# Kernel tuning notes

Hardware: AMD Instinct MI355X
Metric: run time of the kernel (lower is better)

## Reference

```python
import jax, jax.numpy as jnp
import numpy as np

D_MODEL = 1024
EXPAND = 2
D_INNER = D_MODEL * EXPAND  # 2048 independent SSM channels
D_STATE = 16
BATCH = 4
SEQ = 4096


def setup_inputs() -> dict:
    key = jax.random.key(0)
    ks = jax.random.split(key, 10)
    w = lambda k, shape, scale=0.02: jax.random.normal(k, shape, jnp.float32) * scale
    return {
        "x": jax.random.normal(ks[0], (BATCH, SEQ, D_MODEL), jnp.float32),
        "w_in": w(ks[1], (D_MODEL, D_INNER)),
        "b_in": jnp.zeros((D_INNER,), jnp.float32),
        "w_gate": w(ks[2], (D_MODEL, D_INNER)),
        "b_gate": jnp.zeros((D_INNER,), jnp.float32),
        # per-channel linear SSM params: h_t = A h_{t-1} + B x_t ; y_t = C . h_t
        "A": w(ks[3], (D_INNER, D_STATE, D_STATE), 0.05),  # small spectral radius -> stable recurrence
        "B_ssm": w(ks[4], (D_INNER, D_STATE), 0.1),
        "C_ssm": w(ks[5], (D_INNER, D_STATE), 0.1),
        "w_out": w(ks[6], (D_INNER, D_MODEL)),
        "b_out": jnp.zeros((D_MODEL,), jnp.float32),
    }


def reference(x, w_in, b_in, w_gate, b_gate, A, B_ssm, C_ssm, w_out, b_out):
    # x: [B, S, D]
    x_proj = x @ w_in + b_in                     # [B, S, C]
    gate = jax.nn.sigmoid(x @ w_gate + b_gate)   # [B, S, C]

    def step(h, xt):
        # h: [B, C, N] state for all channels; xt: [B, C] scalar input per channel
        h = jnp.einsum("cnm,bcm->bcn", A, h) + B_ssm[None] * xt[:, :, None]
        y = jnp.einsum("bcn,cn->bc", h, C_ssm)
        return h, y

    h0 = jnp.zeros((x.shape[0], D_INNER, D_STATE), x.dtype)
    xs = jnp.swapaxes(x_proj, 0, 1)              # [S, B, C]
    _, ys = jax.lax.scan(step, h0, xs)           # ys: [S, B, C]
    ssm_out = jnp.swapaxes(ys, 0, 1)             # [B, S, C]

    y = ssm_out * gate
    return y @ w_out + b_out                     # [B, S, D]
```

## Files before the change

### kernel.cpp

```cpp
#include <hip/hip_runtime.h>
#include <hip/hip_bf16.h>

#define D_MODEL 1024
#define D_INNER 2048
#define D_STATE 16
#define BATCH   4
#define SEQ     4096
#define MROWS   (BATCH * SEQ)

#define LTAPS 16
#define TSPAN 64

using bf16 = __hip_bfloat16;

typedef __attribute__((ext_vector_type(8))) short bf16x8;
typedef __attribute__((ext_vector_type(4))) float f32x4;

__device__ __forceinline__ float bf2f(bf16 v) { return __bfloat162float(v); }
__device__ __forceinline__ unsigned short f2bfbits(float f) {
  bf16 h = __float2bfloat16(f);
  return *(unsigned short*)&h;
}
__device__ __forceinline__ float bfbits2f(unsigned short u) {
  union { float f; unsigned int i; } x; x.i = (unsigned int)u << 16; return x.f;
}

#define AS1CAST(p) ((const __attribute__((address_space(1))) unsigned int*)(unsigned long long)(p))
#define AS3CAST(p) ((__attribute__((address_space(3))) unsigned int*)(unsigned long long)(p))

#define TILE_E 16384

struct G4 {
  const bf16 *gA, *gB;
  int sW;
  int baseA0, baseA1;
  int baseB0, baseB1;
  int wr, wc, lane;
};

template<int KK>
__device__ __forceinline__ void g4_setup(G4& g, const bf16* A, const bf16* BT,
                                         int m0, int n0)
{
  const int tid = threadIdx.x;
  g.lane = tid & 63;
  const int wv = tid >> 6;
  g.wr = wv >> 1;
  g.wc = wv & 1;
  const int lr = g.lane >> 3, sl = g.lane & 7;
  g.gA = A  + (size_t)(m0 + wv * 64 + lr) * KK + (sl ^ lr) * 8;
  g.gB = BT + (size_t)(n0 + wv * 64 + lr) * KK + (sl ^ lr) * 8;
  g.sW = wv * 4096;
  const int fla = g.lane & 15, cb = g.lane >> 4;
  const int s0 = cb ^ (fla & 7);
  g.baseA0 = (g.wr * 128 + fla) * 64 + s0 * 8;
  g.baseA1 = (g.wr * 128 + fla) * 64 + (s0 ^ 4) * 8;
  g.baseB0 = (g.wc * 128 + fla) * 64 + s0 * 8;
  g.baseB1 = (g.wc * 128 + fla) * 64 + (s0 ^ 4) * 8;
}

template<int KK>
__device__ __forceinline__ void g4_stage(const bf16* s, bf16* d)
{
#pragma unroll
  for (int i = 0; i < 8; ++i)
    __builtin_amdgcn_global_load_lds(AS1CAST(s + (size_t)i * 8 * KK),
                                     AS3CAST(d + i * 512), 16, 0, 0);
}

__device__ __forceinline__ void rd8(bf16x8 (&d)[8], const bf16* T, int base)
{
#pragma unroll
  for (int i = 0; i < 8; ++i)
    d[i] = *(const bf16x8*)&T[base + i * 1024];
}

#define CL64(AF, BF) do { _Pragma("unroll") \
  for (int mi = 0; mi < 8; ++mi) { _Pragma("unroll") \
    for (int ni = 0; ni < 8; ++ni) \
      acc[mi][ni] = __builtin_amdgcn_mfma_f32_16x16x32_bf16( \
          (AF)[mi], (BF)[ni], acc[mi][ni], 0, 0, 0); \
  } } while (0)

template<int KK, int CUR, bool MORE>
__device__ __forceinline__ void g4_tile(const G4& g, bf16* As, bf16* Bs, int t,
    f32x4 (&acc)[8][8],
    bf16x8 (&a0)[8], bf16x8 (&b0)[8], bf16x8 (&a1)[8], bf16x8 (&b1)[8])
{
  const bf16* Ac = As + CUR * TILE_E;
  const bf16* Bc = Bs + CUR * TILE_E;
  rd8(a1, Ac, g.baseA1);
  rd8(b1, Bc, g.baseB1);
  if constexpr (MORE) {
    g4_stage<KK>(g.gA + (size_t)(t + 1) * 64, As + (CUR ^ 1) * TILE_E + g.sW);
    g4_stage<KK>(g.gB + (size_t)(t + 1) * 64, Bs + (CUR ^ 1) * TILE_E + g.sW);
  }
  __builtin_amdgcn_sched_barrier(0);
  CL64(a0, b0);
  __builtin_amdgcn_sched_barrier(0);
  asm volatile("s_waitcnt lgkmcnt(0)" ::: "memory");
  if constexpr (MORE) {
    asm volatile("s_waitcnt vmcnt(0)" ::: "memory");
    __builtin_amdgcn_s_barrier();
    rd8(a0, As + (CUR ^ 1) * TILE_E, g.baseA0);
    rd8(b0, Bs + (CUR ^ 1) * TILE_E, g.baseB0);
  }
  __builtin_amdgcn_sched_barrier(0);
  CL64(a1, b1);
}

template<int KK>
__device__ __forceinline__ void g4_main(const G4& g, bf16* As, bf16* Bs,
                                        f32x4 (&acc)[8][8])
{
  const int nt = KK >> 6;
  g4_stage<KK>(g.gA, As + g.sW);
  g4_stage<KK>(g.gB, Bs + g.sW);
  asm volatile("s_waitcnt vmcnt(0)" ::: "memory");
  __builtin_amdgcn_s_barrier();

  bf16x8 a0[8], b0[8], a1[8], b1[8];
  rd8(a0, As, g.baseA0);
  rd8(b0, Bs, g.baseB0);

  for (int t = 0; t < nt - 2; t += 2) {
    g4_tile<KK, 0, true>(g, As, Bs, t,     acc, a0, b0, a1, b1);
    g4_tile<KK, 1, true>(g, As, Bs, t + 1, acc, a0, b0, a1, b1);
  }
  g4_tile<KK, 0, true >(g, As, Bs, nt - 2, acc, a0, b0, a1, b1);
  g4_tile<KK, 1, false>(g, As, Bs, nt - 1, acc, a0, b0, a1, b1);
}

__global__ __launch_bounds__(256, 1) void gemm_proj_dual(
    const bf16* __restrict__ A,
    const bf16* __restrict__ BT,
    const float* __restrict__ bias_in, const float* __restrict__ bias_gate,
    bf16* __restrict__ xp, bf16* __restrict__ gate)
{
  __shared__ alignas(16) bf16 As[2 * TILE_E];
  __shared__ alignas(16) bf16 Bs[2 * TILE_E];

  const int b = blockIdx.x;
  const int swz = (b & 7) * 128 + (b >> 3);
  const int bm = swz >> 4, bn = swz & 15;
  const int m0 = bm * 256, n0 = bn * 256;

  G4 g;
  g4_setup<D_MODEL>(g, A, BT, m0, n0);

  f32x4 acc[8][8];
#pragma unroll
  for (int i = 0; i < 8; ++i)
#pragma unroll
    for (int j = 0; j < 8; ++j) acc[i][j] = (f32x4){0.f, 0.f, 0.f, 0.f};

  g4_main<D_MODEL>(g, As, Bs, acc);

  const bool isGate = (n0 >= D_INNER);
  const int  nloc0  = n0 - (isGate ? D_INNER : 0);
  const float* bias = isGate ? bias_gate : bias_in;
  bf16* dst         = isGate ? gate : xp;

  const int crow = (g.lane >> 4) * 4;
  const int ccol = g.lane & 15;
#pragma unroll
  for (int mi = 0; mi < 8; ++mi)
#pragma unroll
    for (int ni = 0; ni < 8; ++ni) {
      const int col = nloc0 + g.wc * 128 + ni * 16 + ccol;
      const float bcol = bias[col];
#pragma unroll
      for (int r = 0; r < 4; ++r) {
        const size_t row = (size_t)(m0 + g.wr * 128 + mi * 16 + crow + r);
        float v = acc[mi][ni][r] + bcol;
        if (isGate) v = 1.0f / (1.0f + __expf(-v));
        dst[row * D_INNER + col] = __float2bfloat16(v);
      }
    }
}

__global__ __launch_bounds__(256, 1) void gemm_out(
    const bf16* __restrict__ A,
    const bf16* __restrict__ BT,
    const float* __restrict__ bias,
    float* __restrict__ C)
{
  __shared__ alignas(16) bf16 As[2 * TILE_E];
  __shared__ alignas(16) bf16 Bs[2 * TILE_E];

  const int b = blockIdx.x;
  const int swz = (b & 7) * 32 + (b >> 3);
  const int bm = swz >> 2, bn = swz & 3;
  const int m0 = bm * 256, n0 = bn * 256;

  G4 g;
  g4_setup<D_INNER>(g, A, BT, m0, n0);

  f32x4 acc[8][8];
#pragma unroll
  for (int i = 0; i < 8; ++i)
#pragma unroll
    for (int j = 0; j < 8; ++j) acc[i][j] = (f32x4){0.f, 0.f, 0.f, 0.f};

  g4_main<D_INNER>(g, As, Bs, acc);

  const int crow = (g.lane >> 4) * 4;
  const int ccol = g.lane & 15;
#pragma unroll
  for (int mi = 0; mi < 8; ++mi)
#pragma unroll
    for (int ni = 0; ni < 8; ++ni) {
      const int col = n0 + g.wc * 128 + ni * 16 + ccol;
      const float bcol = bias[col];
#pragma unroll
      for (int r = 0; r < 4; ++r) {
        const size_t row = (size_t)(m0 + g.wr * 128 + mi * 16 + crow + r);
        C[row * D_MODEL + col] = acc[mi][ni][r] + bcol;
      }
    }
}

__global__ __launch_bounds__(256) void f32_to_bf16(
    const float* __restrict__ in, bf16* __restrict__ out, int n4)
{
  const int i = (blockIdx.x * 256 + threadIdx.x);
  if (i >= n4) return;
  const float4 v = *(const float4*)(in + (size_t)i * 4);
  ushort4 r;
  r.x = f2bfbits(v.x); r.y = f2bfbits(v.y); r.z = f2bfbits(v.z); r.w = f2bfbits(v.w);
  *(ushort4*)(out + (size_t)i * 4) = r;
}

__global__ __launch_bounds__(256) void transpose_to_bf16(
    const float* __restrict__ in, bf16* __restrict__ out, int R, int C)
{
  __shared__ float tile[32][33];
  const int c0 = blockIdx.x * 32, r0 = blockIdx.y * 32;
  const int tx = threadIdx.x & 31, ty = threadIdx.x >> 5;
#pragma unroll
  for (int i = ty; i < 32; i += 8)
    tile[i][tx] = in[(size_t)(r0 + i) * C + c0 + tx];
  __syncthreads();
#pragma unroll
  for (int i = ty; i < 32; i += 8)
    out[(size_t)(c0 + i) * R + r0 + tx] = __float2bfloat16(tile[tx][i]);
}

__device__ __forceinline__ float4 load4f(const float* p) { return *(const float4*)p; }

__global__ __launch_bounds__(256) void ssm_taps(
    const float* __restrict__ A, const float* __restrict__ Bv,
    const float* __restrict__ Cv, float* __restrict__ g)
{
  const int c = blockIdx.x * blockDim.x + threadIdx.x;
  if (c >= D_INNER) return;
  const float* Ac = A + (size_t)c * D_STATE * D_STATE;
  float v[D_STATE], cr[D_STATE];
#pragma unroll
  for (int i = 0; i < D_STATE; ++i) {
    v[i]  = Bv[(size_t)c * D_STATE + i];
    cr[i] = Cv[(size_t)c * D_STATE + i];
  }
  for (int m = 0; m < LTAPS; ++m) {
    float y = 0.f;
#pragma unroll
    for (int i = 0; i < D_STATE; ++i) y += cr[i] * v[i];
    g[(size_t)m * D_INNER + c] = y;
    float nv[D_STATE];
#pragma unroll
    for (int n = 0; n < D_STATE; ++n) {
      const float4 a0 = load4f(Ac + n * D_STATE + 0);
      const float4 a1 = load4f(Ac + n * D_STATE + 4);
      const float4 a2 = load4f(Ac + n * D_STATE + 8);
      const float4 a3 = load4f(Ac + n * D_STATE + 12);
      float s = a0.x * v[0] + a0.y * v[1] + a0.z * v[2] + a0.w * v[3];
      s += a1.x * v[4] + a1.y * v[5] + a1.z * v[6] + a1.w * v[7];
      s += a2.x * v[8] + a2.y * v[9] + a2.z * v[10] + a2.w * v[11];
      s += a3.x * v[12] + a3.y * v[13] + a3.z * v[14] + a3.w * v[15];
      nv[n] = s;
    }
#pragma unroll
    for (int i = 0; i < D_STATE; ++i) v[i] = nv[i];
  }
}

__global__ __launch_bounds__(256) void conv_gate(
    const bf16* __restrict__ xp, bf16* __restrict__ gate_io,
    const float* __restrict__ g)
{
  const int cp = blockIdx.x * blockDim.x + threadIdx.x;
  const int c  = cp * 2;
  const int b  = blockIdx.z;
  const int t0 = blockIdx.y * TSPAN;

  float gg0[LTAPS], gg1[LTAPS];
#pragma unroll
  for (int m = 0; m < LTAPS; ++m) {
    gg0[m] = g[(size_t)m * D_INNER + c];
    gg1[m] = g[(size_t)m * D_INNER + c + 1];
  }

  const size_t baseBC = ((size_t)b * SEQ) * D_INNER + c;

  float w0[2 * LTAPS], w1[2 * LTAPS];
#pragma unroll
  for (int j = 0; j < LTAPS; ++j) {
    const int t = t0 - LTAPS + j;
    if (t >= 0) {
      const ushort2 v = *(const ushort2*)&xp[baseBC + (size_t)t * D_INNER];
      w0[j] = bfbits2f(v.x); w1[j] = bfbits2f(v.y);
    } else { w0[j] = 0.f; w1[j] = 0.f; }
  }

  for (int blk = 0; blk < TSPAN; blk += LTAPS) {
#pragma unroll
    for (int j = 0; j < LTAPS; ++j) {
      const ushort2 v = *(const ushort2*)&xp[baseBC + (size_t)(t0 + blk + j) * D_INNER];
      w0[LTAPS + j] = bfbits2f(v.x); w1[LTAPS + j] = bfbits2f(v.y);
    }
#pragma unroll
    for (int j = 0; j < LTAPS; ++j) {
      float y0 = 0.f, y1 = 0.f;
#pragma unroll
      for (int m = 0; m < LTAPS; ++m) {
        y0 += gg0[m] * w0[LTAPS + j - m];
        y1 += gg1[m] * w1[LTAPS + j - m];
      }
      const size_t idx = baseBC + (size_t)(t0 + blk + j) * D_INNER;
      const unsigned int gv = *(const unsigned int*)&gate_io[idx];
      const float g0 = bfbits2f((unsigned short)(gv & 0xffffu));
      const float g1 = bfbits2f((unsigned short)(gv >> 16));
      const unsigned int ov =
          (unsigned int)f2bfbits(y0 * g0) | ((unsigned int)f2bfbits(y1 * g1) << 16);
      *(unsigned int*)&gate_io[idx] = ov;
    }
#pragma unroll
    for (int j = 0; j < LTAPS; ++j) { w0[j] = w0[j + LTAPS]; w1[j] = w1[j + LTAPS]; }
  }
}

extern "C" void kernel_launch(void* const* d_in, const int* in_sizes, int n_in,
                              void* d_out, int out_size, void* d_ws, size_t ws_size,
                              hipStream_t stream)
{
  const float* x      = (const float*)d_in[0];
  const float* w_in   = (const float*)d_in[1];
  const float* b_in   = (const float*)d_in[2];
  const float* w_gate = (const float*)d_in[3];
  const float* b_gate = (const float*)d_in[4];
  const float* A      = (const float*)d_in[5];
  const float* B_ssm  = (const float*)d_in[6];
  const float* C_ssm  = (const float*)d_in[7];
  const float* w_out  = (const float*)d_in[8];
  const float* b_out  = (const float*)d_in[9];
  float* out = (float*)d_out;

  char* ws = (char*)d_ws;
  bf16*  gate  = (bf16*)(ws);
  bf16*  xbf   = (bf16*)(ws + 67108864);
  bf16*  wcatT = (bf16*)(ws + 100663296);
  bf16*  w_otT = (bf16*)(ws + 109051904);
  float* taps  = (float*)(ws + 113246208);
  bf16*  xp    = (bf16*)d_out;

  dim3 blk(256);

  hipLaunchKernelGGL(ssm_taps, dim3(D_INNER / 256), blk, 0, stream, A, B_ssm, C_ssm, taps);
  hipLaunchKernelGGL(f32_to_bf16, dim3((MROWS * D_MODEL / 4) / 256), blk, 0, stream,
                     x, xbf, MROWS * D_MODEL / 4);
  hipLaunchKernelGGL(transpose_to_bf16, dim3(D_INNER / 32, D_MODEL / 32), blk, 0, stream,
                     w_in, wcatT, D_MODEL, D_INNER);
  hipLaunchKernelGGL(transpose_to_bf16, dim3(D_INNER / 32, D_MODEL / 32), blk, 0, stream,
                     w_gate, wcatT + (size_t)D_INNER * D_MODEL, D_MODEL, D_INNER);
  hipLaunchKernelGGL(transpose_to_bf16, dim3(D_MODEL / 32, D_INNER / 32), blk, 0, stream,
                     w_out, w_otT, D_INNER, D_MODEL);

  dim3 gblk(256);
  hipLaunchKernelGGL(gemm_proj_dual, dim3((2 * D_INNER / 256) * (MROWS / 256)), gblk, 0, stream,
                     xbf, wcatT, b_in, b_gate, xp, gate);

  dim3 gc(D_INNER / 2 / 256, SEQ / TSPAN, BATCH);
  hipLaunchKernelGGL(conv_gate, gc, blk, 0, stream, xp, gate, taps);

  hipLaunchKernelGGL(gemm_out, dim3((D_MODEL / 256) * (MROWS / 256)), gblk, 0, stream,
                     gate, w_otT, b_out, out);
}
```

Baseline: 471.5 us.

## Switch GEMMs to 32x32x16 MFMA with 8 waves and fuse prep kernels

Both GEMMs are rewritten to use 512-thread blocks (8 waves, 2x4 layout), each wave computing a 128x64 sub-tile with 32x32x16 bf16 MFMA instead of 16x16x32. The K-tile is split into four 16-wide sub-steps with register double-buffering, and s_setprio is raised around MFMA clusters. The five prep kernels (x cast, three weight transposes, SSM taps) are merged into one launch. The aim is fewer LDS reads per FLOP, more waves to hide latency, and less launch overhead, at the cost of new register and occupancy tradeoffs (launch bounds 512,2) and a new fragment layout in the epilogue.

```diff
diff --git a/kernel.cpp b/kernel.cpp
--- a/kernel.cpp
+++ b/kernel.cpp
@@ -13,8 +13,8 @@
 
 using bf16 = __hip_bfloat16;
 
-typedef __attribute__((ext_vector_type(8))) short bf16x8;
-typedef __attribute__((ext_vector_type(4))) float f32x4;
+typedef __attribute__((ext_vector_type(8)))  short bf16x8;
+typedef __attribute__((ext_vector_type(16))) float f32x16;
 
 __device__ __forceinline__ float bf2f(bf16 v) { return __bfloat162float(v); }
 __device__ __forceinline__ unsigned short f2bfbits(float f) {
@@ -28,110 +28,133 @@
 #define AS1CAST(p) ((const __attribute__((address_space(1))) unsigned int*)(unsigned long long)(p))
 #define AS3CAST(p) ((__attribute__((address_space(3))) unsigned int*)(unsigned long long)(p))
 
+#define PRIO1 __builtin_amdgcn_s_setprio(1)
+#define PRIO0 __builtin_amdgcn_s_setprio(0)
+#define SBAR0 __builtin_amdgcn_sched_barrier(0)
+
 #define TILE_E 16384
 
-struct G4 {
+struct G32 {
   const bf16 *gA, *gB;
+  size_t K64, K128;
   int sW;
-  int baseA0, baseA1;
-  int baseB0, baseB1;
-  int wr, wc, lane;
+  int offA[4], offB[4];
+  int wm, wn, lane;
 };
 
 template<int KK>
-__device__ __forceinline__ void g4_setup(G4& g, const bf16* A, const bf16* BT,
-                                         int m0, int n0)
+__device__ __forceinline__ void g32_setup(G32& g, const bf16* A, const bf16* BT,
+                                          int m0, int n0)
 {
   const int tid = threadIdx.x;
   g.lane = tid & 63;
   const int wv = tid >> 6;
-  g.wr = wv >> 1;
-  g.wc = wv & 1;
+  g.wm = wv >> 2;
+  g.wn = wv & 3;
   const int lr = g.lane >> 3, sl = g.lane & 7;
-  g.gA = A  + (size_t)(m0 + wv * 64 + lr) * KK + (sl ^ lr) * 8;
-  g.gB = BT + (size_t)(n0 + wv * 64 + lr) * KK + (sl ^ lr) * 8;
-  g.sW = wv * 4096;
-  const int fla = g.lane & 15, cb = g.lane >> 4;
-  const int s0 = cb ^ (fla & 7);
-  g.baseA0 = (g.wr * 128 + fla) * 64 + s0 * 8;
-  g.baseA1 = (g.wr * 128 + fla) * 64 + (s0 ^ 4) * 8;
-  g.baseB0 = (g.wc * 128 + fla) * 64 + s0 * 8;
-  g.baseB1 = (g.wc * 128 + fla) * 64 + (s0 ^ 4) * 8;
-}
-
-template<int KK>
-__device__ __forceinline__ void g4_stage(const bf16* s, bf16* d)
-{
-#pragma unroll
-  for (int i = 0; i < 8; ++i)
-    __builtin_amdgcn_global_load_lds(AS1CAST(s + (size_t)i * 8 * KK),
-                                     AS3CAST(d + i * 512), 16, 0, 0);
-}
-
-__device__ __forceinline__ void rd8(bf16x8 (&d)[8], const bf16* T, int base)
-{
-#pragma unroll
-  for (int i = 0; i < 8; ++i)
-    d[i] = *(const bf16x8*)&T[base + i * 1024];
-}
-
-#define CL64(AF, BF) do { _Pragma("unroll") \
-  for (int mi = 0; mi < 8; ++mi) { _Pragma("unroll") \
-    for (int ni = 0; ni < 8; ++ni) \
-      acc[mi][ni] = __builtin_amdgcn_mfma_f32_16x16x32_bf16( \
-          (AF)[mi], (BF)[ni], acc[mi][ni], 0, 0, 0); \
+  g.gA = A  + (size_t)(m0 + wv * 8 + lr) * KK + (sl ^ lr) * 8;
+  g.gB = BT + (size_t)(n0 + wv * 8 + lr) * KK + (sl ^ lr) * 8;
+  g.K64  = (size_t)64 * KK;
+  g.K128 = (size_t)128 * KK;
+  g.sW = wv * 8 * 64;
+  const int l31 = g.lane & 31, hi = g.lane >> 5;
+#pragma unroll
+  for (int ks = 0; ks < 4; ++ks) {
+    const int slot = ((ks * 2 + hi) ^ (l31 & 7)) * 8;
+    g.offA[ks] = (g.wm * 128 + l31) * 64 + slot;
+    g.offB[ks] = (g.wn * 64  + l31) * 64 + slot;
+  }
+}
+
+__device__ __forceinline__ void g32_stage2(const bf16* s, bf16* d, size_t K64)
+{
+  __builtin_amdgcn_global_load_lds(AS1CAST(s),       AS3CAST(d),        16, 0, 0);
+  __builtin_amdgcn_global_load_lds(AS1CAST(s + K64), AS3CAST(d + 4096), 16, 0, 0);
+}
+
+__device__ __forceinline__ void rdA32(bf16x8 (&d)[4], const bf16* T, int off)
+{
+#pragma unroll
+  for (int am = 0; am < 4; ++am) d[am] = *(const bf16x8*)&T[off + am * 2048];
+}
+__device__ __forceinline__ void rdB32(bf16x8 (&d)[2], const bf16* T, int off)
+{
+#pragma unroll
+  for (int bn = 0; bn < 2; ++bn) d[bn] = *(const bf16x8*)&T[off + bn * 2048];
+}
+
+#define CL8(AF, BF) do { _Pragma("unroll") \
+  for (int am = 0; am < 4; ++am) { _Pragma("unroll") \
+    for (int bn = 0; bn < 2; ++bn) \
+      acc[am][bn] = __builtin_amdgcn_mfma_f32_32x32x16_bf16( \
+          (AF)[am], (BF)[bn], acc[am][bn], 0, 0, 0); \
   } } while (0)
 
-template<int KK, int CUR, bool MORE>
-__device__ __forceinline__ void g4_tile(const G4& g, bf16* As, bf16* Bs, int t,
-    f32x4 (&acc)[8][8],
-    bf16x8 (&a0)[8], bf16x8 (&b0)[8], bf16x8 (&a1)[8], bf16x8 (&b1)[8])
-{
-  const bf16* Ac = As + CUR * TILE_E;
-  const bf16* Bc = Bs + CUR * TILE_E;
-  rd8(a1, Ac, g.baseA1);
-  rd8(b1, Bc, g.baseB1);
+template<bool MORE>
+__device__ __forceinline__ void g32_tile(const G32& g, bf16* As, bf16* Bs, int t,
+    f32x16 (&acc)[4][2], bf16x8 (&aC)[4], bf16x8 (&bC)[2],
+    bf16x8 (&aN)[4], bf16x8 (&bN)[2])
+{
+  const int cur = t & 1;
+  const bf16* Ac = As + cur * TILE_E;
+  const bf16* Bc = Bs + cur * TILE_E;
+  bf16* Anx = As + (cur ^ 1) * TILE_E;
+  bf16* Bnx = Bs + (cur ^ 1) * TILE_E;
+
+  rdA32(aN, Ac, g.offA[1]);
+  rdB32(bN, Bc, g.offB[1]);
   if constexpr (MORE) {
-    g4_stage<KK>(g.gA + (size_t)(t + 1) * 64, As + (CUR ^ 1) * TILE_E + g.sW);
-    g4_stage<KK>(g.gB + (size_t)(t + 1) * 64, Bs + (CUR ^ 1) * TILE_E + g.sW);
-  }
-  __builtin_amdgcn_sched_barrier(0);
-  CL64(a0, b0);
-  __builtin_amdgcn_sched_barrier(0);
-  asm volatile("s_waitcnt lgkmcnt(0)" ::: "memory");
+    const size_t tau = (size_t)(t + 1) * 64;
+    g32_stage2(g.gA + tau,           Anx + g.sW,        g.K64);
+    g32_stage2(g.gA + g.K128 + tau,  Anx + 8192 + g.sW, g.K64);
+    g32_stage2(g.gB + tau,           Bnx + g.sW,        g.K64);
+    g32_stage2(g.gB + g.K128 + tau,  Bnx + 8192 + g.sW, g.K64);
+  }
+  SBAR0;
+  PRIO1; CL8(aC, bC); PRIO0;
+  rdA32(aC, Ac, g.offA[2]);
+  rdB32(bC, Bc, g.offB[2]);
+  SBAR0;
+  PRIO1; CL8(aN, bN); PRIO0;
+  rdA32(aN, Ac, g.offA[3]);
+  rdB32(bN, Bc, g.offB[3]);
+  SBAR0;
+  PRIO1; CL8(aC, bC); PRIO0;
   if constexpr (MORE) {
+    asm volatile("s_waitcnt lgkmcnt(0)" ::: "memory");
     asm volatile("s_waitcnt vmcnt(0)" ::: "memory");
     __builtin_amdgcn_s_barrier();
-    rd8(a0, As + (CUR ^ 1) * TILE_E, g.baseA0);
-    rd8(b0, Bs + (CUR ^ 1) * TILE_E, g.baseB0);
-  }
-  __builtin_amdgcn_sched_barrier(0);
-  CL64(a1, b1);
+  }
+  SBAR0;
+  PRIO1; CL8(aN, bN); PRIO0;
+  if constexpr (MORE) {
+    rdA32(aC, Anx, g.offA[0]);
+    rdB32(bC, Bnx, g.offB[0]);
+  }
 }
 
 template<int KK>
-__device__ __forceinline__ void g4_main(const G4& g, bf16* As, bf16* Bs,
-                                        f32x4 (&acc)[8][8])
+__device__ __forceinline__ void g32_main(const G32& g, bf16* As, bf16* Bs,
+                                         f32x16 (&acc)[4][2])
 {
   const int nt = KK >> 6;
-  g4_stage<KK>(g.gA, As + g.sW);
-  g4_stage<KK>(g.gB, Bs + g.sW);
+  g32_stage2(g.gA,           As + g.sW,        g.K64);
+  g32_stage2(g.gA + g.K128,  As + 8192 + g.sW, g.K64);
+  g32_stage2(g.gB,           Bs + g.sW,        g.K64);
+  g32_stage2(g.gB + g.K128,  Bs + 8192 + g.sW, g.K64);
   asm volatile("s_waitcnt vmcnt(0)" ::: "memory");
   __builtin_amdgcn_s_barrier();
 
-  bf16x8 a0[8], b0[8], a1[8], b1[8];
-  rd8(a0, As, g.baseA0);
-  rd8(b0, Bs, g.baseB0);
-
-  for (int t = 0; t < nt - 2; t += 2) {
-    g4_tile<KK, 0, true>(g, As, Bs, t,     acc, a0, b0, a1, b1);
-    g4_tile<KK, 1, true>(g, As, Bs, t + 1, acc, a0, b0, a1, b1);
-  }
-  g4_tile<KK, 0, true >(g, As, Bs, nt - 2, acc, a0, b0, a1, b1);
-  g4_tile<KK, 1, false>(g, As, Bs, nt - 1, acc, a0, b0, a1, b1);
-}
-
-__global__ __launch_bounds__(256, 1) void gemm_proj_dual(
+  bf16x8 aC[4], bC[2], aN[4], bN[2];
+  rdA32(aC, As, g.offA[0]);
+  rdB32(bC, Bs, g.offB[0]);
+
+  for (int t = 0; t < nt - 1; ++t)
+    g32_tile<true>(g, As, Bs, t, acc, aC, bC, aN, bN);
+  g32_tile<false>(g, As, Bs, nt - 1, acc, aC, bC, aN, bN);
+}
+
+__global__ __launch_bounds__(512, 2) void gemm_proj_dual(
     const bf16* __restrict__ A,
     const bf16* __restrict__ BT,
     const float* __restrict__ bias_in, const float* __restrict__ bias_gate,
@@ -145,41 +168,43 @@
   const int bm = swz >> 4, bn = swz & 15;
   const int m0 = bm * 256, n0 = bn * 256;
 
-  G4 g;
-  g4_setup<D_MODEL>(g, A, BT, m0, n0);
-
-  f32x4 acc[8][8];
-#pragma unroll
-  for (int i = 0; i < 8; ++i)
-#pragma unroll
-    for (int j = 0; j < 8; ++j) acc[i][j] = (f32x4){0.f, 0.f, 0.f, 0.f};
-
-  g4_main<D_MODEL>(g, As, Bs, acc);
+  G32 g;
+  g32_setup<D_MODEL>(g, A, BT, m0, n0);
+
+  f32x16 acc[4][2];
+#pragma unroll
+  for (int i = 0; i < 4; ++i)
+#pragma unroll
+    for (int j = 0; j < 2; ++j)
+#pragma unroll
+      for (int r = 0; r < 16; ++r) acc[i][j][r] = 0.f;
+
+  g32_main<D_MODEL>(g, As, Bs, acc);
 
   const bool isGate = (n0 >= D_INNER);
   const int  nloc0  = n0 - (isGate ? D_INNER : 0);
   const float* bias = isGate ? bias_gate : bias_in;
   bf16* dst         = isGate ? gate : xp;
 
-  const int crow = (g.lane >> 4) * 4;
-  const int ccol = g.lane & 15;
-#pragma unroll
-  for (int mi = 0; mi < 8; ++mi)
-#pragma unroll
-    for (int ni = 0; ni < 8; ++ni) {
-      const int col = nloc0 + g.wc * 128 + ni * 16 + ccol;
+  const int l31 = g.lane & 31, hi = g.lane >> 5;
+#pragma unroll
+  for (int am = 0; am < 4; ++am)
+#pragma unroll
+    for (int bn2 = 0; bn2 < 2; ++bn2) {
+      const int col = nloc0 + g.wn * 64 + bn2 * 32 + l31;
       const float bcol = bias[col];
 #pragma unroll
-      for (int r = 0; r < 4; ++r) {
-        const size_t row = (size_t)(m0 + g.wr * 128 + mi * 16 + crow + r);
-        float v = acc[mi][ni][r] + bcol;
+      for (int reg = 0; reg < 16; ++reg) {
+        const int rowl = (reg & 3) + 8 * (reg >> 2) + 4 * hi;
+        const size_t row = (size_t)(m0 + g.wm * 128 + am * 32 + rowl);
+        float v = acc[am][bn2][reg] + bcol;
         if (isGate) v = 1.0f / (1.0f + __expf(-v));
         dst[row * D_INNER + col] = __float2bfloat16(v);
       }
     }
 }
 
-__global__ __launch_bounds__(256, 1) void gemm_out(
+__global__ __launch_bounds__(512, 2) void gemm_out(
     const bf16* __restrict__ A,
     const bf16* __restrict__ BT,
     const float* __restrict__ bias,
@@ -193,49 +218,43 @@
   const int bm = swz >> 2, bn = swz & 3;
   const int m0 = bm * 256, n0 = bn * 256;
 
-  G4 g;
-  g4_setup<D_INNER>(g, A, BT, m0, n0);
-
-  f32x4 acc[8][8];
-#pragma unroll
-  for (int i = 0; i < 8; ++i)
-#pragma unroll
-    for (int j = 0; j < 8; ++j) acc[i][j] = (f32x4){0.f, 0.f, 0.f, 0.f};
-
-  g4_main<D_INNER>(g, As, Bs, acc);
-
-  const int crow = (g.lane >> 4) * 4;
-  const int ccol = g.lane & 15;
-#pragma unroll
-  for (int mi = 0; mi < 8; ++mi)
-#pragma unroll
-    for (int ni = 0; ni < 8; ++ni) {
-      const int col = n0 + g.wc * 128 + ni * 16 + ccol;
+  G32 g;
+  g32_setup<D_INNER>(g, A, BT, m0, n0);
+
+  f32x16 acc[4][2];
+#pragma unroll
+  for (int i = 0; i < 4; ++i)
+#pragma unroll
+    for (int j = 0; j < 2; ++j)
+#pragma unroll
+      for (int r = 0; r < 16; ++r) acc[i][j][r] = 0.f;
+
+  g32_main<D_INNER>(g, As, Bs, acc);
+
+  const int l31 = g.lane & 31, hi = g.lane >> 5;
+#pragma unroll
+  for (int am = 0; am < 4; ++am)
+#pragma unroll
+    for (int bn2 = 0; bn2 < 2; ++bn2) {
+      const int col = n0 + g.wn * 64 + bn2 * 32 + l31;
       const float bcol = bias[col];
 #pragma unroll
-      for (int r = 0; r < 4; ++r) {
-        const size_t row = (size_t)(m0 + g.wr * 128 + mi * 16 + crow + r);
-        C[row * D_MODEL + col] = acc[mi][ni][r] + bcol;
+      for (int reg = 0; reg < 16; ++reg) {
+        const int rowl = (reg & 3) + 8 * (reg >> 2) + 4 * hi;
+        const size_t row = (size_t)(m0 + g.wm * 128 + am * 32 + rowl);
+        C[row * D_MODEL + col] = acc[am][bn2][reg] + bcol;
       }
     }
 }
 
-__global__ __launch_bounds__(256) void f32_to_bf16(
-    const float* __restrict__ in, bf16* __restrict__ out, int n4)
-{
-  const int i = (blockIdx.x * 256 + threadIdx.x);
-  if (i >= n4) return;
-  const float4 v = *(const float4*)(in + (size_t)i * 4);
-  ushort4 r;
-  r.x = f2bfbits(v.x); r.y = f2bfbits(v.y); r.z = f2bfbits(v.z); r.w = f2bfbits(v.w);
-  *(ushort4*)(out + (size_t)i * 4) = r;
-}
-
-__global__ __launch_bounds__(256) void transpose_to_bf16(
-    const float* __restrict__ in, bf16* __restrict__ out, int R, int C)
-{
-  __shared__ float tile[32][33];
-  const int c0 = blockIdx.x * 32, r0 = blockIdx.y * 32;
+__device__ __forceinline__ float4 load4f(const float* p) { return *(const float4*)p; }
+
+__device__ __forceinline__ void transpose_body(
+    const float* __restrict__ in, bf16* __restrict__ out, int R, int C,
+    int idx, float (*tile)[33])
+{
+  const int nbx = C / 32;
+  const int c0 = (idx % nbx) * 32, r0 = (idx / nbx) * 32;
   const int tx = threadIdx.x & 31, ty = threadIdx.x >> 5;
 #pragma unroll
   for (int i = ty; i < 32; i += 8)
@@ -246,41 +265,61 @@
     out[(size_t)(c0 + i) * R + r0 + tx] = __float2bfloat16(tile[tx][i]);
 }
 
-__device__ __forceinline__ float4 load4f(const float* p) { return *(const float4*)p; }
-
-__global__ __launch_bounds__(256) void ssm_taps(
+__global__ __launch_bounds__(256) void prep_all(
+    const float* __restrict__ x,
+    const float* __restrict__ w_in, const float* __restrict__ w_gate,
+    const float* __restrict__ w_out,
     const float* __restrict__ A, const float* __restrict__ Bv,
-    const float* __restrict__ Cv, float* __restrict__ g)
-{
-  const int c = blockIdx.x * blockDim.x + threadIdx.x;
-  if (c >= D_INNER) return;
-  const float* Ac = A + (size_t)c * D_STATE * D_STATE;
-  float v[D_STATE], cr[D_STATE];
-#pragma unroll
-  for (int i = 0; i < D_STATE; ++i) {
-    v[i]  = Bv[(size_t)c * D_STATE + i];
-    cr[i] = Cv[(size_t)c * D_STATE + i];
-  }
-  for (int m = 0; m < LTAPS; ++m) {
-    float y = 0.f;
-#pragma unroll
-    for (int i = 0; i < D_STATE; ++i) y += cr[i] * v[i];
-    g[(size_t)m * D_INNER + c] = y;
-    float nv[D_STATE];
-#pragma unroll
-    for (int n = 0; n < D_STATE; ++n) {
-      const float4 a0 = load4f(Ac + n * D_STATE + 0);
-      const float4 a1 = load4f(Ac + n * D_STATE + 4);
-      const float4 a2 = load4f(Ac + n * D_STATE + 8);
-      const float4 a3 = load4f(Ac + n * D_STATE + 12);
-      float s = a0.x * v[0] + a0.y * v[1] + a0.z * v[2] + a0.w * v[3];
-      s += a1.x * v[4] + a1.y * v[5] + a1.z * v[6] + a1.w * v[7];
-      s += a2.x * v[8] + a2.y * v[9] + a2.z * v[10] + a2.w * v[11];
-      s += a3.x * v[12] + a3.y * v[13] + a3.z * v[14] + a3.w * v[15];
-      nv[n] = s;
-    }
-#pragma unroll
-    for (int i = 0; i < D_STATE; ++i) v[i] = nv[i];
+    const float* __restrict__ Cv,
+    bf16* __restrict__ xbf, bf16* __restrict__ wcatT,
+    bf16* __restrict__ w_otT, float* __restrict__ taps)
+{
+  __shared__ float tile[32][33];
+  const int bid = blockIdx.x;
+  if (bid < 16384) {
+    const int i = bid * 256 + threadIdx.x;
+    const float4 v = *(const float4*)(x + (size_t)i * 4);
+    ushort4 r;
+    r.x = f2bfbits(v.x); r.y = f2bfbits(v.y); r.z = f2bfbits(v.z); r.w = f2bfbits(v.w);
+    *(ushort4*)(xbf + (size_t)i * 4) = r;
+  } else if (bid < 18432) {
+    transpose_body(w_in, wcatT, D_MODEL, D_INNER, bid - 16384, tile);
+  } else if (bid < 20480) {
+    transpose_body(w_gate, wcatT + (size_t)D_INNER * D_MODEL, D_MODEL, D_INNER,
+                   bid - 18432, tile);
+  } else if (bid < 22528) {
+    transpose_body(w_out, w_otT, D_INNER, D_MODEL, bid - 20480, tile);
+  } else {
+    const int c = (bid - 22528) * 256 + threadIdx.x;
+    if (c >= D_INNER) return;
+    const float* Ac = A + (size_t)c * D_STATE * D_STATE;
+    float v[D_STATE], cr[D_STATE];
+#pragma unroll
+    for (int i = 0; i < D_STATE; ++i) {
+      v[i]  = Bv[(size_t)c * D_STATE + i];
+      cr[i] = Cv[(size_t)c * D_STATE + i];
+    }
+    for (int m = 0; m < LTAPS; ++m) {
+      float y = 0.f;
+#pragma unroll
+      for (int i = 0; i < D_STATE; ++i) y += cr[i] * v[i];
+      taps[(size_t)m * D_INNER + c] = y;
+      float nv[D_STATE];
+#pragma unroll
+      for (int n = 0; n < D_STATE; ++n) {
+        const float4 a0 = load4f(Ac + n * D_STATE + 0);
+        const float4 a1 = load4f(Ac + n * D_STATE + 4);
+        const float4 a2 = load4f(Ac + n * D_STATE + 8);
+        const float4 a3 = load4f(Ac + n * D_STATE + 12);
+        float s = a0.x * v[0] + a0.y * v[1] + a0.z * v[2] + a0.w * v[3];
+        s += a1.x * v[4] + a1.y * v[5] + a1.z * v[6] + a1.w * v[7];
+        s += a2.x * v[8] + a2.y * v[9] + a2.z * v[10] + a2.w * v[11];
+        s += a3.x * v[12] + a3.y * v[13] + a3.z * v[14] + a3.w * v[15];
+        nv[n] = s;
+      }
+#pragma unroll
+      for (int i = 0; i < D_STATE; ++i) v[i] = nv[i];
+    }
   }
 }
 
@@ -363,24 +402,16 @@
   float* taps  = (float*)(ws + 113246208);
   bf16*  xp    = (bf16*)d_out;
 
-  dim3 blk(256);
-
-  hipLaunchKernelGGL(ssm_taps, dim3(D_INNER / 256), blk, 0, stream, A, B_ssm, C_ssm, taps);
-  hipLaunchKernelGGL(f32_to_bf16, dim3((MROWS * D_MODEL / 4) / 256), blk, 0, stream,
-                     x, xbf, MROWS * D_MODEL / 4);
-  hipLaunchKernelGGL(transpose_to_bf16, dim3(D_INNER / 32, D_MODEL / 32), blk, 0, stream,
-                     w_in, wcatT, D_MODEL, D_INNER);
-  hipLaunchKernelGGL(transpose_to_bf16, dim3(D_INNER / 32, D_MODEL / 32), blk, 0, stream,
-                     w_gate, wcatT + (size_t)D_INNER * D_MODEL, D_MODEL, D_INNER);
-  hipLaunchKernelGGL(transpose_to_bf16, dim3(D_MODEL / 32, D_INNER / 32), blk, 0, stream,
-                     w_out, w_otT, D_INNER, D_MODEL);
-
-  dim3 gblk(256);
+  hipLaunchKernelGGL(prep_all, dim3(22536), dim3(256), 0, stream,
+                     x, w_in, w_gate, w_out, A, B_ssm, C_ssm,
+                     xbf, wcatT, w_otT, taps);
+
+  dim3 gblk(512);
   hipLaunchKernelGGL(gemm_proj_dual, dim3((2 * D_INNER / 256) * (MROWS / 256)), gblk, 0, stream,
                      xbf, wcatT, b_in, b_gate, xp, gate);
 
   dim3 gc(D_INNER / 2 / 256, SEQ / TSPAN, BATCH);
-  hipLaunchKernelGGL(conv_gate, gc, blk, 0, stream, xp, gate, taps);
+  hipLaunchKernelGGL(conv_gate, gc, dim3(256), 0, stream, xp, gate, taps);
 
   hipLaunchKernelGGL(gemm_out, dim3((D_MODEL / 256) * (MROWS / 256)), gblk, 0, stream,
                      gate, w_otT, b_out, out);
```

After: 491.6 us. 1.04x slower.
